# Optimization experiments

Hardware: AMD Instinct MI355X
Metric: run time of the kernel (lower is better)

The kernel has to match this reference:

```python
import jax, jax.numpy as jnp
import numpy as np

ORDER = 2
M = 3  # number_timeseries


def setup_inputs() -> dict:
    key = jax.random.key(0)
    ks = jax.random.split(key, 8)
    N, T = 256, 4096
    H, OUT = 128, 10
    d_phi_in = (ORDER + 1) * M          # 9
    d_rho_in = ORDER * M + H            # 134
    s = lambda fan_in: 1.0 / np.sqrt(fan_in)
    return {
        "x": jax.random.normal(ks[0], (N, M * T), dtype=jnp.float32),
        "phi_w1": jax.random.normal(ks[1], (d_phi_in, H), dtype=jnp.float32) * s(d_phi_in),
        "phi_b1": jnp.zeros((H,), jnp.float32),
        "phi_w2": jax.random.normal(ks[2], (H, H), dtype=jnp.float32) * s(H),
        "phi_b2": jnp.zeros((H,), jnp.float32),
        "phi_w3": jax.random.normal(ks[3], (H, H), dtype=jnp.float32) * s(H),
        "phi_b3": jnp.zeros((H,), jnp.float32),
        "rho_w1": jax.random.normal(ks[4], (d_rho_in, H), dtype=jnp.float32) * s(d_rho_in),
        "rho_b1": jnp.zeros((H,), jnp.float32),
        "rho_w2": jax.random.normal(ks[5], (H, OUT), dtype=jnp.float32) * s(H),
        "rho_b2": jnp.zeros((OUT,), jnp.float32),
    }


def reference(x, phi_w1, phi_b1, phi_w2, phi_b2, phi_w3, phi_b3,
              rho_w1, rho_b1, rho_w2, rho_b2):
    N = x.shape[0]
    xr = x.reshape(N, M, -1)                      # (N, M, T)
    T = xr.shape[-1]
    L = T - ORDER                                 # number of windows
    # cat over lags along channel dim, then transpose -> (N, L, (ORDER+1)*M)
    input_inner = jnp.concatenate(
        [xr[:, :, i:L + i] for i in range(ORDER + 1)], axis=1
    ).swapaxes(1, 2)                              # (N, L, 9)
    h = jax.nn.relu(input_inner @ phi_w1 + phi_b1)
    h = jax.nn.relu(h @ phi_w2 + phi_b2)
    h = h @ phi_w3 + phi_b3                       # (N, L, 128)
    output_inner = jnp.sum(h, axis=1)             # (N, 128)
    input_outer = jnp.concatenate(
        [xr[:, :, :ORDER].reshape(N, -1), output_inner], axis=1
    )                                             # (N, 134)
    g = jax.nn.relu(input_outer @ rho_w1 + rho_b1)
    return g @ rho_w2 + rho_b2                    # (N, 10)
```

## Files before the change

kernel.cpp:

```cpp
#include <hip/hip_runtime.h>
#include <hip/hip_bf16.h>


#define NN 256
#define MM 3
#define TT 4096
#define LL 4094
#define HH 128
#define CHUNKS 8
#define RPC 512
#define STEPS 8
#define SR 64

typedef __attribute__((ext_vector_type(8))) short bf16x8;
typedef __attribute__((ext_vector_type(4))) float f32x4;
typedef __attribute__((ext_vector_type(4))) unsigned short u16x4;

__device__ __forceinline__ unsigned short f2bf(float x) {
    union { float f; unsigned u; } v; v.f = x;
    unsigned r = v.u + 0x7fffu + ((v.u >> 16) & 1u);
    return (unsigned short)(r >> 16);
}

__global__ __launch_bounds__(256, 2) void pen_inner(
    const float* __restrict__ x,
    const float* __restrict__ w1, const float* __restrict__ b1,
    const float* __restrict__ w2, const float* __restrict__ b2,
    float* __restrict__ partials)
{
    __shared__ __align__(16) float xw[RPC * 12];
    __shared__ __align__(16) unsigned short h1s[SR * HH];

    const int tid  = threadIdx.x;
    const int wave = tid >> 6;
    const int lane = tid & 63;
    const int lr   = lane & 15;
    const int lq   = lane >> 4;

    const int bx    = blockIdx.x;
    const int n     = bx >> 3;
    const int chunk = bx & 7;
    const int l0c   = chunk * RPC;

    const float* xn = x + n * (MM * TT);
    for (int idx = tid; idx < RPC * 9; idx += 256) {
        int r = idx / 9;
        int k = idx - r * 9;
        int i = k / 3;
        int m = k - i * 3;
        int t = l0c + r + i;
        xw[r * 12 + k] = (t < TT) ? xn[m * TT + t] : 0.f;
    }

    const int fo0 = wave * 2;
    bf16x8 w1f[2];
    bf16x8 w2f[2][4];
    float  b2v[2][4];
    #pragma unroll
    for (int f = 0; f < 2; ++f) {
        const int c = (fo0 + f) * 16 + lr;
        bf16x8 a;
        #pragma unroll
        for (int e = 0; e < 8; ++e) {
            int k = lq * 8 + e;
            float v = 0.f;
            if (k < 9)       v = w1[k * HH + c];
            else if (k == 9) v = b1[c];
            a[e] = (short)f2bf(v);
        }
        w1f[f] = a;
        #pragma unroll
        for (int kk = 0; kk < 4; ++kk) {
            bf16x8 wv;
            #pragma unroll
            for (int e = 0; e < 8; ++e) {
                int i = kk * 32 + lq * 8 + e;
                wv[e] = (short)f2bf(w2[i * HH + c]);
            }
            w2f[f][kk] = wv;
        }
        #pragma unroll
        for (int j = 0; j < 4; ++j) b2v[f][j] = b2[(fo0 + f) * 16 + lq * 4 + j];
    }

    float colsum[2][4] = {{0.f,0.f,0.f,0.f},{0.f,0.f,0.f,0.f}};
    const f32x4 zero4 = {0.f, 0.f, 0.f, 0.f};

    for (int s = 0; s < STEPS; ++s) {
        __syncthreads();

        f32x4 acc1[2][4];
        #pragma unroll
        for (int rf = 0; rf < 4; ++rf) {
            const int r = s * SR + rf * 16 + lr;
            bf16x8 bfrag;
            #pragma unroll
            for (int e = 0; e < 8; ++e) bfrag[e] = 0;
            if (lq == 0) {
                f32x4 lo = *(const f32x4*)&xw[r * 12];
                f32x4 hi = *(const f32x4*)&xw[r * 12 + 4];
                #pragma unroll
                for (int e = 0; e < 4; ++e) bfrag[e]     = (short)f2bf(lo[e]);
                #pragma unroll
                for (int e = 0; e < 4; ++e) bfrag[4 + e] = (short)f2bf(hi[e]);
            } else if (lq == 1) {
                bfrag[0] = (short)f2bf(xw[r * 12 + 8]);
                bfrag[1] = (short)0x3F80;
            }
            #pragma unroll
            for (int f = 0; f < 2; ++f)
                acc1[f][rf] = __builtin_amdgcn_mfma_f32_16x16x32_bf16(
                                  w1f[f], bfrag, zero4, 0, 0, 0);
        }

        #pragma unroll
        for (int rf = 0; rf < 4; ++rf) {
            const int r   = rf * 16 + lr;
            const int swz = (r & 7) << 3;
            #pragma unroll
            for (int f = 0; f < 2; ++f) {
                const int cbase = (fo0 + f) * 16 + lq * 4;
                u16x4 pk;
                #pragma unroll
                for (int j = 0; j < 4; ++j)
                    pk[j] = f2bf(fmaxf(acc1[f][rf][j], 0.f));
                *(u16x4*)&h1s[r * HH + (cbase ^ swz)] = pk;
            }
        }
        __syncthreads();

        f32x4 acc2[2][4];
        #pragma unroll
        for (int f = 0; f < 2; ++f)
            #pragma unroll
            for (int rf = 0; rf < 4; ++rf) acc2[f][rf] = zero4;

        #pragma unroll
        for (int rf = 0; rf < 4; ++rf) {
            const int r   = rf * 16 + lr;
            const int swz = (r & 7) << 3;
            bf16x8 hf[4];
            #pragma unroll
            for (int kk = 0; kk < 4; ++kk) {
                const int ibase = kk * 32 + lq * 8;
                hf[kk] = *(const bf16x8*)&h1s[r * HH + (ibase ^ swz)];
            }
            #pragma unroll
            for (int f = 0; f < 2; ++f)
                #pragma unroll
                for (int kk = 0; kk < 4; ++kk)
                    acc2[f][rf] = __builtin_amdgcn_mfma_f32_16x16x32_bf16(
                                      w2f[f][kk], hf[kk], acc2[f][rf], 0, 0, 0);
        }

        #pragma unroll
        for (int rf = 0; rf < 4; ++rf) {
            const bool valid = (l0c + s * SR + rf * 16 + lr) < LL;
            #pragma unroll
            for (int f = 0; f < 2; ++f)
                #pragma unroll
                for (int j = 0; j < 4; ++j) {
                    float v = fmaxf(acc2[f][rf][j] + b2v[f][j], 0.f);
                    if (valid) colsum[f][j] += v;
                }
        }
    }

    #pragma unroll
    for (int f = 0; f < 2; ++f)
        #pragma unroll
        for (int j = 0; j < 4; ++j) {
            float v = colsum[f][j];
            #pragma unroll
            for (int msk = 1; msk < 16; msk <<= 1)
                v += __shfl_xor(v, msk, 64);
            if (lr == 0) {
                const int o = (fo0 + f) * 16 + lq * 4 + j;
                partials[(n * CHUNKS + chunk) * HH + o] = v;
            }
        }
}

__global__ __launch_bounds__(128) void pen_outer(
    const float* __restrict__ x,
    const float* __restrict__ w3, const float* __restrict__ b3,
    const float* __restrict__ rw1, const float* __restrict__ rb1,
    const float* __restrict__ rw2, const float* __restrict__ rb2,
    const float* __restrict__ partials,
    float* __restrict__ out)
{
    __shared__ float S[HH];
    __shared__ float IO[136];
    __shared__ float G[HH];
    const int n = blockIdx.x;
    const int c = threadIdx.x;

    float s = 0.f;
    #pragma unroll
    for (int ch = 0; ch < CHUNKS; ++ch)
        s += partials[(n * CHUNKS + ch) * HH + c];
    S[c] = s;
    if (c < 6) IO[c] = x[n * (MM * TT) + (c >> 1) * TT + (c & 1)];
    __syncthreads();

    float oi = (float)LL * b3[c];
    for (int k = 0; k < HH; ++k) oi += S[k] * w3[k * HH + c];
    IO[6 + c] = oi;
    __syncthreads();

    float g = rb1[c];
    for (int k = 0; k < 134; ++k) g += IO[k] * rw1[k * HH + c];
    G[c] = fmaxf(g, 0.f);
    __syncthreads();

    if (c < 10) {
        float o = rb2[c];
        for (int k = 0; k < HH; ++k) o += G[k] * rw2[k * 10 + c];
        out[n * 10 + c] = o;
    }
}

extern "C" void kernel_launch(void* const* d_in, const int* in_sizes, int n_in,
                              void* d_out, int out_size, void* d_ws, size_t ws_size,
                              hipStream_t stream)
{
    (void)in_sizes; (void)n_in; (void)out_size; (void)ws_size;
    const float* x   = (const float*)d_in[0];
    const float* w1  = (const float*)d_in[1];
    const float* b1  = (const float*)d_in[2];
    const float* w2  = (const float*)d_in[3];
    const float* b2  = (const float*)d_in[4];
    const float* w3  = (const float*)d_in[5];
    const float* b3  = (const float*)d_in[6];
    const float* rw1 = (const float*)d_in[7];
    const float* rb1 = (const float*)d_in[8];
    const float* rw2 = (const float*)d_in[9];
    const float* rb2 = (const float*)d_in[10];

    float* partials = (float*)d_ws;

    pen_inner<<<NN * CHUNKS, 256, 0, stream>>>(x, w1, b1, w2, b2, partials);
    pen_outer<<<NN, 128, 0, stream>>>(x, w3, b3, rw1, rb1, rw2, rb2, partials,
                                      (float*)d_out);
}
```

Baseline: 86.81 us.

## Pre-convert inputs to bf16 in LDS, fold biases into MFMA accumulators, raise occupancy

The window buffer in shared memory now holds bf16 values in MFMA fragment layout, so each row fragment is a single 16-byte LDS load with no per-step conversion or lane branching. Both biases are passed as the initial MFMA accumulator instead of using a ones-column and separate adds. The validity mask is only evaluated on the last step of the last chunk, h1 packing uses 32-bit words, and launch bounds ask for 4 blocks per CU. The higher occupancy target may force register spilling, and the hardware bf16 conversion must round the same way as before.

```diff
diff --git a/kernel.cpp b/kernel.cpp
--- a/kernel.cpp
+++ b/kernel.cpp
@@ -15,20 +15,21 @@
 typedef __attribute__((ext_vector_type(8))) short bf16x8;
 typedef __attribute__((ext_vector_type(4))) float f32x4;
 typedef __attribute__((ext_vector_type(4))) unsigned short u16x4;
+typedef __attribute__((ext_vector_type(2))) unsigned int u32x2;
 
 __device__ __forceinline__ unsigned short f2bf(float x) {
-    union { float f; unsigned u; } v; v.f = x;
-    unsigned r = v.u + 0x7fffu + ((v.u >> 16) & 1u);
-    return (unsigned short)(r >> 16);
-}
-
-__global__ __launch_bounds__(256, 2) void pen_inner(
+    __hip_bfloat16 h = __float2bfloat16(x);
+    union { __hip_bfloat16 h; unsigned short u; } v; v.h = h;
+    return v.u;
+}
+
+__global__ __launch_bounds__(256, 4) void pen_inner(
     const float* __restrict__ x,
     const float* __restrict__ w1, const float* __restrict__ b1,
     const float* __restrict__ w2, const float* __restrict__ b2,
     float* __restrict__ partials)
 {
-    __shared__ __align__(16) float xw[RPC * 12];
+    __shared__ __align__(16) unsigned short xw[RPC * 16 + 64];
     __shared__ __align__(16) unsigned short h1s[SR * HH];
 
     const int tid  = threadIdx.x;
@@ -43,19 +44,31 @@
     const int l0c   = chunk * RPC;
 
     const float* xn = x + n * (MM * TT);
-    for (int idx = tid; idx < RPC * 9; idx += 256) {
-        int r = idx / 9;
-        int k = idx - r * 9;
-        int i = k / 3;
-        int m = k - i * 3;
-        int t = l0c + r + i;
-        xw[r * 12 + k] = (t < TT) ? xn[m * TT + t] : 0.f;
-    }
+
+    #pragma unroll
+    for (int k = 0; k < 8; ++k) {
+        const int i = k / 3;
+        const int m = k - i * 3;
+        for (int r = tid; r < RPC; r += 256) {
+            int t = l0c + r + i;
+            float v = (t < TT) ? xn[m * TT + t] : 0.f;
+            xw[r * 16 + k] = f2bf(v);
+        }
+    }
+    for (int r = tid; r < RPC; r += 256) {
+        int t = l0c + r + 2;
+        float v = (t < TT) ? xn[2 * TT + t] : 0.f;
+        u16x4 a; a[0] = f2bf(v); a[1] = 0; a[2] = 0; a[3] = 0;
+        u16x4 z; z[0] = 0; z[1] = 0; z[2] = 0; z[3] = 0;
+        *(u16x4*)&xw[r * 16 + 8]  = a;
+        *(u16x4*)&xw[r * 16 + 12] = z;
+    }
+    if (tid < 64) xw[RPC * 16 + tid] = 0;
 
     const int fo0 = wave * 2;
     bf16x8 w1f[2];
     bf16x8 w2f[2][4];
-    float  b2v[2][4];
+    f32x4  b1f[2], b2f[2];
     #pragma unroll
     for (int f = 0; f < 2; ++f) {
         const int c = (fo0 + f) * 16 + lr;
@@ -63,28 +76,25 @@
         #pragma unroll
         for (int e = 0; e < 8; ++e) {
             int k = lq * 8 + e;
-            float v = 0.f;
-            if (k < 9)       v = w1[k * HH + c];
-            else if (k == 9) v = b1[c];
-            a[e] = (short)f2bf(v);
+            a[e] = (short)((k < 9) ? f2bf(w1[k * HH + c]) : (unsigned short)0);
         }
         w1f[f] = a;
         #pragma unroll
         for (int kk = 0; kk < 4; ++kk) {
             bf16x8 wv;
             #pragma unroll
-            for (int e = 0; e < 8; ++e) {
-                int i = kk * 32 + lq * 8 + e;
-                wv[e] = (short)f2bf(w2[i * HH + c]);
-            }
+            for (int e = 0; e < 8; ++e)
+                wv[e] = (short)f2bf(w2[(kk * 32 + lq * 8 + e) * HH + c]);
             w2f[f][kk] = wv;
         }
         #pragma unroll
-        for (int j = 0; j < 4; ++j) b2v[f][j] = b2[(fo0 + f) * 16 + lq * 4 + j];
+        for (int j = 0; j < 4; ++j) {
+            b1f[f][j] = b1[(fo0 + f) * 16 + lq * 4 + j];
+            b2f[f][j] = b2[(fo0 + f) * 16 + lq * 4 + j];
+        }
     }
 
     float colsum[2][4] = {{0.f,0.f,0.f,0.f},{0.f,0.f,0.f,0.f}};
-    const f32x4 zero4 = {0.f, 0.f, 0.f, 0.f};
 
     for (int s = 0; s < STEPS; ++s) {
         __syncthreads();
@@ -93,24 +103,9 @@
         #pragma unroll
         for (int rf = 0; rf < 4; ++rf) {
             const int r = s * SR + rf * 16 + lr;
-            bf16x8 bfrag;
-            #pragma unroll
-            for (int e = 0; e < 8; ++e) bfrag[e] = 0;
-            if (lq == 0) {
-                f32x4 lo = *(const f32x4*)&xw[r * 12];
-                f32x4 hi = *(const f32x4*)&xw[r * 12 + 4];
-                #pragma unroll
-                for (int e = 0; e < 4; ++e) bfrag[e]     = (short)f2bf(lo[e]);
-                #pragma unroll
-                for (int e = 0; e < 4; ++e) bfrag[4 + e] = (short)f2bf(hi[e]);
-            } else if (lq == 1) {
-                bfrag[0] = (short)f2bf(xw[r * 12 + 8]);
-                bfrag[1] = (short)0x3F80;
-            }
-            #pragma unroll
-            for (int f = 0; f < 2; ++f)
-                acc1[f][rf] = __builtin_amdgcn_mfma_f32_16x16x32_bf16(
-                                  w1f[f], bfrag, zero4, 0, 0, 0);
+            bf16x8 bfrag = *(const bf16x8*)&xw[r * 16 + lq * 8];
+            acc1[0][rf] = __builtin_amdgcn_mfma_f32_16x16x32_bf16(w1f[0], bfrag, b1f[0], 0, 0, 0);
+            acc1[1][rf] = __builtin_amdgcn_mfma_f32_16x16x32_bf16(w1f[1], bfrag, b1f[1], 0, 0, 0);
         }
 
         #pragma unroll
@@ -119,50 +114,56 @@
             const int swz = (r & 7) << 3;
             #pragma unroll
             for (int f = 0; f < 2; ++f) {
-                const int cbase = (fo0 + f) * 16 + lq * 4;
-                u16x4 pk;
-                #pragma unroll
-                for (int j = 0; j < 4; ++j)
-                    pk[j] = f2bf(fmaxf(acc1[f][rf][j], 0.f));
-                *(u16x4*)&h1s[r * HH + (cbase ^ swz)] = pk;
+                const int cb = (fo0 + f) * 16 + lq * 4;
+                unsigned p0 = f2bf(fmaxf(acc1[f][rf][0], 0.f));
+                unsigned p1 = f2bf(fmaxf(acc1[f][rf][1], 0.f));
+                unsigned p2 = f2bf(fmaxf(acc1[f][rf][2], 0.f));
+                unsigned p3 = f2bf(fmaxf(acc1[f][rf][3], 0.f));
+                u32x2 pk;
+                pk[0] = p0 | (p1 << 16);
+                pk[1] = p2 | (p3 << 16);
+                *(u32x2*)&h1s[r * HH + (cb ^ swz)] = pk;
             }
         }
         __syncthreads();
 
         f32x4 acc2[2][4];
-        #pragma unroll
-        for (int f = 0; f < 2; ++f)
-            #pragma unroll
-            for (int rf = 0; rf < 4; ++rf) acc2[f][rf] = zero4;
-
         #pragma unroll
         for (int rf = 0; rf < 4; ++rf) {
             const int r   = rf * 16 + lr;
             const int swz = (r & 7) << 3;
             bf16x8 hf[4];
             #pragma unroll
-            for (int kk = 0; kk < 4; ++kk) {
-                const int ibase = kk * 32 + lq * 8;
-                hf[kk] = *(const bf16x8*)&h1s[r * HH + (ibase ^ swz)];
-            }
-            #pragma unroll
-            for (int f = 0; f < 2; ++f)
+            for (int kk = 0; kk < 4; ++kk)
+                hf[kk] = *(const bf16x8*)&h1s[r * HH + ((kk * 32 + lq * 8) ^ swz)];
+            acc2[0][rf] = __builtin_amdgcn_mfma_f32_16x16x32_bf16(w2f[0][0], hf[0], b2f[0], 0, 0, 0);
+            acc2[1][rf] = __builtin_amdgcn_mfma_f32_16x16x32_bf16(w2f[1][0], hf[0], b2f[1], 0, 0, 0);
+            #pragma unroll
+            for (int kk = 1; kk < 4; ++kk) {
+                acc2[0][rf] = __builtin_amdgcn_mfma_f32_16x16x32_bf16(w2f[0][kk], hf[kk], acc2[0][rf], 0, 0, 0);
+                acc2[1][rf] = __builtin_amdgcn_mfma_f32_16x16x32_bf16(w2f[1][kk], hf[kk], acc2[1][rf], 0, 0, 0);
+            }
+        }
+
+        const bool tailstep = (chunk == CHUNKS - 1) && (s == STEPS - 1);
+        #pragma unroll
+        for (int rf = 0; rf < 4; ++rf) {
+            if (tailstep && rf == 3) {
+                const bool valid = lr < 14;
                 #pragma unroll
-                for (int kk = 0; kk < 4; ++kk)
-                    acc2[f][rf] = __builtin_amdgcn_mfma_f32_16x16x32_bf16(
-                                      w2f[f][kk], hf[kk], acc2[f][rf], 0, 0, 0);
-        }
-
-        #pragma unroll
-        for (int rf = 0; rf < 4; ++rf) {
-            const bool valid = (l0c + s * SR + rf * 16 + lr) < LL;
-            #pragma unroll
-            for (int f = 0; f < 2; ++f)
+                for (int f = 0; f < 2; ++f)
+                    #pragma unroll
+                    for (int j = 0; j < 4; ++j) {
+                        float v = fmaxf(acc2[f][rf][j], 0.f);
+                        if (valid) colsum[f][j] += v;
+                    }
+            } else {
                 #pragma unroll
-                for (int j = 0; j < 4; ++j) {
-                    float v = fmaxf(acc2[f][rf][j] + b2v[f][j], 0.f);
-                    if (valid) colsum[f][j] += v;
-                }
+                for (int f = 0; f < 2; ++f)
+                    #pragma unroll
+                    for (int j = 0; j < 4; ++j)
+                        colsum[f][j] += fmaxf(acc2[f][rf][j], 0.f);
+            }
         }
     }
 
```

Result: faster. 73.01 us (-15.9%).
